# Kernel optimization log

Hardware: AMD Instinct MI355X
Metric: run time of the kernel (lower is better)

## Reference

```python
import jax, jax.numpy as jnp
import numpy as np
from jax import lax

NUM_HEADS = 8
HEAD_DIM = 32
DIM = NUM_HEADS * HEAD_DIM  # 256
SR = 2
B, H, W = 4, 64, 64


def setup_inputs() -> dict:
    key = jax.random.key(0)
    ks = jax.random.split(key, 6)
    x = jax.random.normal(ks[0], (B, DIM, H, W), dtype=jnp.float32)
    # query: 1x1 conv without bias -> plain [out,in] matrix
    Wq = jax.random.normal(ks[1], (DIM, DIM), dtype=jnp.float32) * (1.0 / np.sqrt(DIM))
    # key/value: sr x sr conv, stride sr, no bias (OIHW)
    Wk = jax.random.normal(ks[2], (DIM, DIM, SR, SR), dtype=jnp.float32) * (1.0 / np.sqrt(DIM * SR * SR))
    Wv = jax.random.normal(ks[3], (DIM, DIM, SR, SR), dtype=jnp.float32) * (1.0 / np.sqrt(DIM * SR * SR))
    rel_h = jax.random.normal(ks[4], (1, NUM_HEADS, HEAD_DIM, 1, H // SR), dtype=jnp.float32)
    rel_w = jax.random.normal(ks[5], (1, NUM_HEADS, HEAD_DIM, W // SR, 1), dtype=jnp.float32)
    return {"x": x, "Wq": Wq, "Wk": Wk, "Wv": Wv, "rel_h": rel_h, "rel_w": rel_w}


def reference(x, Wq, Wk, Wv, rel_h, rel_w):
    b, c, h, w = x.shape
    nh, hd = NUM_HEADS, HEAD_DIM
    scale = hd ** (-0.5)
    dn = ('NCHW', 'OIHW', 'NCHW')

    # q: 1x1 conv == channel matmul; [B, C, H*W] -> [B, nh, hd, Nq]
    q = jnp.einsum('oc,bchw->bohw', Wq, x).reshape(b, nh, hd, h * w)
    # k, v: sr x sr conv, stride sr -> [B, nh, hd, Nkv]
    k = lax.conv_general_dilated(x, Wk, window_strides=(SR, SR), padding='VALID',
                                 dimension_numbers=dn).reshape(b, nh, hd, -1)
    v = lax.conv_general_dilated(x, Wv, window_strides=(SR, SR), padding='VALID',
                                 dimension_numbers=dn).reshape(b, nh, hd, -1)

    # attn scores: q^T k -> [B, nh, Nq, Nkv]
    attn = jnp.einsum('bhdn,bhdm->bhnm', q, k)
    # relative positional bias: (rel_h + rel_w) broadcast -> [nh, hd, Nkv]
    pos = (rel_h + rel_w).reshape(nh, hd, -1)
    attn = attn + jnp.einsum('bhdn,hdm->bhnm', q, pos)
    attn = jax.nn.softmax(attn * scale, axis=-1)

    # out = v @ attn^T -> [B, nh, hd, Nq] -> [B, C, H, W]
    out = jnp.einsum('bhdm,bhnm->bhdn', v, attn).reshape(b, c, h, w)
    return out
```

## Files before the change

kernel.cpp:

```cpp
#include <hip/hip_runtime.h>
#include <math.h>


typedef __bf16 bf16;
typedef __attribute__((ext_vector_type(4))) __bf16 bf16x4;
typedef __attribute__((ext_vector_type(8))) __bf16 bf16x8;
typedef __attribute__((ext_vector_type(4))) float f32x4;
typedef __attribute__((ext_vector_type(2))) __fp16 fp16x2_raw;
typedef __attribute__((ext_vector_type(4))) _Float16 f16x4;

#define MFMA16 __builtin_amdgcn_mfma_f32_16x16x32_bf16
#define MFMA16H __builtin_amdgcn_mfma_f32_16x16x16f16

#define QSCALE 0.25503486f
#define SOFTMAX_SHIFT 10.0f

__global__ void k_prep_w(const float* __restrict__ Wq, const float* __restrict__ Wk,
                         const float* __restrict__ Wv,
                         bf16* __restrict__ Wq_bf, bf16* __restrict__ Wkv_bf) {
    int tid = blockIdx.x * 256 + threadIdx.x;
    int c = tid >> 8, i = tid & 255;
    const float* Wsrc = (c < 256) ? Wk : Wv;
    int cs = c & 255;
    f32x4 w4 = ((const f32x4*)Wsrc)[cs * 256 + i];
#pragma unroll
    for (int tap = 0; tap < 4; tap++)
        Wkv_bf[c * 1024 + tap * 256 + i] = (bf16)w4[tap];
    if (tid < 16384) {
        f32x4 q4 = ((const f32x4*)Wq)[tid];
        bf16x4 o;
#pragma unroll
        for (int e = 0; e < 4; e++) o[e] = (bf16)(q4[e] * QSCALE);
        *(bf16x4*)(Wq_bf + tid * 4) = o;
    }
}

__global__ void k_xT(const float* __restrict__ x, bf16* __restrict__ xT) {
    int b = blockIdx.z, c0 = blockIdx.y * 64, n0 = blockIdx.x * 64;
    __shared__ float tile[64][65];
    int t = threadIdx.x;
    const float* xp = x + (size_t)(b * 256 + c0) * 4096 + n0;
#pragma unroll
    for (int k2 = 0; k2 < 16; k2++) {
        int flat = k2 * 256 + t;
        int row = flat >> 6, col = flat & 63;
        tile[row][col] = xp[(size_t)row * 4096 + col];
    }
    __syncthreads();
    bf16* op = xT + (size_t)(b * 4096 + n0) * 256 + c0;
#pragma unroll
    for (int k2 = 0; k2 < 16; k2++) {
        int flat = k2 * 256 + t;
        int row = flat >> 6, col = flat & 63;
        op[(size_t)row * 256 + col] = (bf16)tile[col][row];
    }
}

__launch_bounds__(256)
__global__ void k_gemm_kv(const bf16* __restrict__ xT, const bf16* __restrict__ Wkv_bf,
                          const float* __restrict__ rel_h, const float* __restrict__ rel_w,
                          bf16* __restrict__ kpos_t, _Float16* __restrict__ v_td) {
    int b = blockIdx.z;
    int bx = blockIdx.x;
    int m0 = bx * 32;
    int c0w = blockIdx.y * 64 + (threadIdx.x >> 6) * 16;
    int t = threadIdx.x, l = t & 63;
    int lr = l & 15, lg = l >> 4;
    __shared__ __align__(16) bf16 Ps[2][32 * 264];
    const bf16* xb = xT + (size_t)b * 4096 * 256;
    int srow = t >> 3;
    int scu0 = (t & 7) * 4;
    uint4 pre[4];
#define LOAD_CHUNK(tap)                                                        \
    {                                                                          \
        int dy = (tap) >> 1, dx = (tap) & 1;                                   \
        const bf16* src = xb + (size_t)((2 * bx + dy) * 64 + 2 * srow + dx) * 256; \
        _Pragma("unroll")                                                      \
        for (int j = 0; j < 4; j++)                                            \
            pre[j] = *(const uint4*)(src + (scu0 + j) * 8);                    \
    }
#define WRITE_CHUNK(buf)                                                       \
    {                                                                          \
        bf16* dst = Ps[buf] + srow * 264 + scu0 * 8;                           \
        _Pragma("unroll")                                                      \
        for (int j = 0; j < 4; j++) *(uint4*)(dst + j * 8) = pre[j];           \
    }
    LOAD_CHUNK(0)
    WRITE_CHUNK(0)
    const bf16* Gkb = Wkv_bf + (size_t)(c0w + lr) * 1024 + lg * 8;
    const bf16* Gvb = Gkb + 256 * 1024;
    f32x4 accK[2] = {}, accV[2] = {};
    for (int ch = 0; ch < 4; ch++) {
        if (ch < 3) LOAD_CHUNK(ch + 1)
        __syncthreads();
        const bf16* P = Ps[ch & 1];
#pragma unroll
        for (int kk = 0; kk < 8; kk++) {
            bf16x8 pa0 = *(const bf16x8*)(P + lr * 264 + kk * 32 + lg * 8);
            bf16x8 pa1 = *(const bf16x8*)(P + (16 + lr) * 264 + kk * 32 + lg * 8);
            bf16x8 gk = *(const bf16x8*)(Gkb + ch * 256 + kk * 32);
            bf16x8 gv = *(const bf16x8*)(Gvb + ch * 256 + kk * 32);
            accK[0] = MFMA16(pa0, gk, accK[0], 0, 0, 0);
            accK[1] = MFMA16(pa1, gk, accK[1], 0, 0, 0);
            accV[0] = MFMA16(gv, pa0, accV[0], 0, 0, 0);
            accV[1] = MFMA16(gv, pa1, accV[1], 0, 0, 0);
        }
        if (ch < 3) {
            __syncthreads();
            WRITE_CHUNK((ch + 1) & 1)
        }
    }
    {
        int cc = c0w + lr;
        float rw = rel_w[cc * 32 + bx];
#pragma unroll
        for (int i = 0; i < 2; i++)
#pragma unroll
            for (int r = 0; r < 4; r++) {
                int ml = i * 16 + lg * 4 + r;
                float val = accK[i][r] + rw + rel_h[cc * 32 + ml];
                kpos_t[((size_t)(b * 8 + (cc >> 5)) * 1024 + m0 + ml) * 32 + (cc & 31)] = (bf16)val;
            }
    }
#pragma unroll
    for (int j = 0; j < 2; j++) {
        int m = m0 + j * 16 + lr;
#pragma unroll
        for (int r = 0; r < 4; r++) {
            int cc = c0w + lg * 4 + r;
            v_td[((size_t)(b * 8 + (cc >> 5)) * 32 + (cc & 31)) * 1024 + m] = (_Float16)accV[j][r];
        }
    }
#undef LOAD_CHUNK
#undef WRITE_CHUNK
}

__launch_bounds__(512, 8)
__global__ void k_attn(const bf16* __restrict__ xT, const bf16* __restrict__ Wq_bf,
                       const bf16* __restrict__ kpos_t, const _Float16* __restrict__ v_td,
                       float* __restrict__ out) {
    int b = blockIdx.z, h = blockIdx.y;
    int t = threadIdx.x;
    int w = t >> 6, l = t & 63;
    int n0 = blockIdx.x * 128 + w * 16;
    int lr = l & 15, lg = l >> 4;
    const size_t bh = (size_t)(b * 8 + h);
    __shared__ __align__(16) char smem[2 * 128 * 32 * 2 + 2 * 32 * 136 * 2];
    bf16* KsB = (bf16*)smem;
    _Float16* VsB = (_Float16*)(smem + 16384);
    const bf16* Kb = kpos_t + bh * 1024 * 32;
    const _Float16* Vb = v_td + bh * 32 * 1024;
    uint4 pk_r, pv_r;
#define LOADCH(ch)                                                             \
    {                                                                          \
        pk_r = ((const uint4*)(Kb + (size_t)(ch) * 128 * 32))[t];              \
        pv_r = *(const uint4*)(Vb + (size_t)(t >> 4) * 1024 + (ch) * 128 +     \
                               (t & 15) * 8);                                  \
    }
#define WRITECH(buf)                                                           \
    {                                                                          \
        int m = t >> 2;                                                        \
        int phys = ((m >> 1) + (t & 3)) & 3;                                   \
        *(uint4*)(&KsB[(buf) * 4096 + m * 32 + phys * 8]) = pk_r;              \
        *(uint4*)(&VsB[(buf) * (32 * 136) + (t >> 4) * 136 + (t & 15) * 8]) = pv_r; \
    }
    LOADCH(0)
    bf16* Qs = (bf16*)smem + w * 1280;
    bf16x8 bq0;
    {
        const bf16* Aw = Wq_bf + (size_t)(h * 32 + lr) * 256 + lg * 8;
        const bf16* Bx = xT + (size_t)(b * 4096 + n0 + lr) * 256 + lg * 8;
        f32x4 aq[2] = {};
#pragma unroll
        for (int kk = 0; kk < 8; kk++) {
            bf16x8 a0 = *(const bf16x8*)(Aw + kk * 32);
            bf16x8 a1 = *(const bf16x8*)(Aw + 16 * 256 + kk * 32);
            bf16x8 b0 = *(const bf16x8*)(Bx + kk * 32);
            aq[0] = MFMA16(a0, b0, aq[0], 0, 0, 0);
            aq[1] = MFMA16(a1, b0, aq[1], 0, 0, 0);
        }
#pragma unroll
        for (int i = 0; i < 2; i++) {
            bf16x4 pk;
#pragma unroll
            for (int r = 0; r < 4; r++) pk[r] = (bf16)aq[i][r];
            *(bf16x4*)(Qs + lr * 40 + i * 16 + lg * 4) = pk;
        }
        bf16x4 a0 = *(const bf16x4*)(Qs + lr * 40 + lg * 8);
        bf16x4 a1 = *(const bf16x4*)(Qs + lr * 40 + lg * 8 + 4);
#pragma unroll
        for (int e = 0; e < 4; e++) { bq0[e] = a0[e]; bq0[4 + e] = a1[e]; }
    }
    __syncthreads();
    WRITECH(0)
    LOADCH(1)
    __syncthreads();
    f32x4 accO[2] = {};
    f32x4 accS = {};
    const f16x4 onesv = {(_Float16)1.f, (_Float16)1.f, (_Float16)1.f, (_Float16)1.f};
    const f32x4 zs = {-SOFTMAX_SHIFT, -SOFTMAX_SHIFT, -SOFTMAX_SHIFT, -SOFTMAX_SHIFT};
    const int koff = (((lr >> 1) + lg) & 3) * 8;
    for (int ch = 0; ch < 8; ch++) {
        const bf16* Kc = KsB + (ch & 1) * 4096;
        const _Float16* Vc = VsB + (ch & 1) * (32 * 136);
        __builtin_amdgcn_s_setprio(1);
#pragma unroll
        for (int tt = 0; tt < 8; tt++) {
            bf16x8 ak = *(const bf16x8*)(Kc + (tt * 16 + lr) * 32 + koff);
            f32x4 s0 = MFMA16(ak, bq0, zs, 0, 0, 0);
            f16x4 p0;
            {
                fp16x2_raw c01 = __builtin_amdgcn_cvt_pkrtz(
                    __builtin_amdgcn_exp2f(s0[0]), __builtin_amdgcn_exp2f(s0[1]));
                fp16x2_raw c23 = __builtin_amdgcn_cvt_pkrtz(
                    __builtin_amdgcn_exp2f(s0[2]), __builtin_amdgcn_exp2f(s0[3]));
                p0[0] = c01[0]; p0[1] = c01[1]; p0[2] = c23[0]; p0[3] = c23[1];
            }
            f16x4 v0 = *(const f16x4*)(Vc + lr * 136 + tt * 16 + lg * 4);
            f16x4 v1 = *(const f16x4*)(Vc + (16 + lr) * 136 + tt * 16 + lg * 4);
            accO[0] = MFMA16H(p0, v0, accO[0], 0, 0, 0);
            accO[1] = MFMA16H(p0, v1, accO[1], 0, 0, 0);
            accS    = MFMA16H(p0, onesv, accS, 0, 0, 0);
        }
        __builtin_amdgcn_s_setprio(0);
        if (ch < 7) {
            WRITECH((ch + 1) & 1)
            if (ch < 6) LOADCH(ch + 2)
            __syncthreads();
        }
    }
#undef LOADCH
#undef WRITECH
    float inv[4];
#pragma unroll
    for (int r = 0; r < 4; r++) inv[r] = 1.0f / accS[r];
#pragma unroll
    for (int dt = 0; dt < 2; dt++) {
        int c = h * 32 + dt * 16 + lr;
        float* op = out + (size_t)(b * 256 + c) * 4096 + n0 + lg * 4;
        f32x4 o;
#pragma unroll
        for (int r = 0; r < 4; r++) o[r] = accO[dt][r] * inv[r];
        *(f32x4*)op = o;
    }
}

extern "C" void kernel_launch(void* const* d_in, const int* in_sizes, int n_in,
                              void* d_out, int out_size, void* d_ws, size_t ws_size,
                              hipStream_t stream) {
    const float* x    = (const float*)d_in[0];
    const float* Wq   = (const float*)d_in[1];
    const float* Wk   = (const float*)d_in[2];
    const float* Wv   = (const float*)d_in[3];
    const float* relh = (const float*)d_in[4];
    const float* relw = (const float*)d_in[5];
    float* out = (float*)d_out;
    char* ws = (char*)d_ws;

    bf16*      xT     = (bf16*)(ws);
    bf16*      kposT  = (bf16*)(ws + (8u << 20));
    _Float16*  v_td   = (_Float16*)(ws + (10u << 20));
    bf16*      Wq_bf  = (bf16*)(ws + (12u << 20));
    bf16*      Wkv_bf = (bf16*)(ws + (12u << 20) + (256u << 10));

    k_prep_w <<<512,            256, 0, stream>>>(Wq, Wk, Wv, Wq_bf, Wkv_bf);
    k_xT     <<<dim3(64, 4, 4), 256, 0, stream>>>(x, xT);
    k_gemm_kv<<<dim3(32, 4, 4), 256, 0, stream>>>(xT, Wkv_bf, relh, relw, kposT, v_td);
    k_attn   <<<dim3(32, 8, 4), 512, 0, stream>>>(xT, Wq_bf, kposT, v_td, out);
}
```

Measured before the change: 146.5 us.

## Vectorize prep and transpose memory ops, halve gemm_kv tile for more blocks

```diff
diff --git a/kernel.cpp b/kernel.cpp
--- a/kernel.cpp
+++ b/kernel.cpp
@@ -19,19 +19,28 @@
                          const float* __restrict__ Wv,
                          bf16* __restrict__ Wq_bf, bf16* __restrict__ Wkv_bf) {
     int tid = blockIdx.x * 256 + threadIdx.x;
-    int c = tid >> 8, i = tid & 255;
-    const float* Wsrc = (c < 256) ? Wk : Wv;
-    int cs = c & 255;
-    f32x4 w4 = ((const f32x4*)Wsrc)[cs * 256 + i];
-#pragma unroll
-    for (int tap = 0; tap < 4; tap++)
-        Wkv_bf[c * 1024 + tap * 256 + i] = (bf16)w4[tap];
-    if (tid < 16384) {
-        f32x4 q4 = ((const f32x4*)Wq)[tid];
+    if (tid < 32768) {
+        int c = tid >> 6, i4 = (tid & 63) * 4;
+        const float* Wsrc = (c < 256) ? Wk : Wv;
+        int cs = c & 255;
+        f32x4 r[4];
+#pragma unroll
+        for (int j = 0; j < 4; j++)
+            r[j] = ((const f32x4*)Wsrc)[cs * 256 + i4 + j];
+#pragma unroll
+        for (int tap = 0; tap < 4; tap++) {
+            bf16x4 o;
+#pragma unroll
+            for (int j = 0; j < 4; j++) o[j] = (bf16)r[j][tap];
+            *(bf16x4*)(Wkv_bf + c * 1024 + tap * 256 + i4) = o;
+        }
+    } else {
+        int q = tid - 32768;
+        f32x4 q4 = ((const f32x4*)Wq)[q];
         bf16x4 o;
 #pragma unroll
         for (int e = 0; e < 4; e++) o[e] = (bf16)(q4[e] * QSCALE);
-        *(bf16x4*)(Wq_bf + tid * 4) = o;
+        *(bf16x4*)(Wq_bf + q * 4) = o;
     }
 }
 
@@ -41,18 +50,23 @@
     int t = threadIdx.x;
     const float* xp = x + (size_t)(b * 256 + c0) * 4096 + n0;
 #pragma unroll
-    for (int k2 = 0; k2 < 16; k2++) {
-        int flat = k2 * 256 + t;
-        int row = flat >> 6, col = flat & 63;
-        tile[row][col] = xp[(size_t)row * 4096 + col];
+    for (int it = 0; it < 4; it++) {
+        int u = it * 256 + t;
+        int row = u >> 4, colq = u & 15;
+        f32x4 v = *(const f32x4*)(xp + (size_t)row * 4096 + colq * 4);
+#pragma unroll
+        for (int e = 0; e < 4; e++) tile[row][colq * 4 + e] = v[e];
     }
     __syncthreads();
     bf16* op = xT + (size_t)(b * 4096 + n0) * 256 + c0;
 #pragma unroll
-    for (int k2 = 0; k2 < 16; k2++) {
-        int flat = k2 * 256 + t;
-        int row = flat >> 6, col = flat & 63;
-        op[(size_t)row * 256 + col] = (bf16)tile[col][row];
+    for (int it = 0; it < 2; it++) {
+        int u = it * 256 + t;
+        int orow = u >> 3, oc8 = (u & 7) * 8;
+        bf16x8 o;
+#pragma unroll
+        for (int e = 0; e < 8; e++) o[e] = (bf16)tile[oc8 + e][orow];
+        *(bf16x8*)(op + (size_t)orow * 256 + oc8) = o;
     }
 }
 
@@ -62,48 +76,46 @@
                           bf16* __restrict__ kpos_t, _Float16* __restrict__ v_td) {
     int b = blockIdx.z;
     int bx = blockIdx.x;
-    int m0 = bx * 32;
+    int m0 = bx * 16;
     int c0w = blockIdx.y * 64 + (threadIdx.x >> 6) * 16;
     int t = threadIdx.x, l = t & 63;
     int lr = l & 15, lg = l >> 4;
-    __shared__ __align__(16) bf16 Ps[2][32 * 264];
+    __shared__ __align__(16) bf16 Ps[2][16 * 264];
     const bf16* xb = xT + (size_t)b * 4096 * 256;
-    int srow = t >> 3;
-    int scu0 = (t & 7) * 4;
-    uint4 pre[4];
+    int srow = t >> 4;
+    int scu0 = (t & 15) * 2;
+    uint4 pre[2];
 #define LOAD_CHUNK(tap)                                                        \
     {                                                                          \
         int dy = (tap) >> 1, dx = (tap) & 1;                                   \
-        const bf16* src = xb + (size_t)((2 * bx + dy) * 64 + 2 * srow + dx) * 256; \
+        const bf16* src = xb + (size_t)((2 * (bx >> 1) + dy) * 64 +            \
+                                        2 * ((bx & 1) * 16 + srow) + dx) * 256;\
         _Pragma("unroll")                                                      \
-        for (int j = 0; j < 4; j++)                                            \
-            pre[j] = *(const uint4*)(src + (scu0 + j) * 8);                    \
+        for (int j = 0; j < 2; j++)                                            \
+            pre[j] = ((const uint4*)src)[scu0 + j];                            \
     }
 #define WRITE_CHUNK(buf)                                                       \
     {                                                                          \
         bf16* dst = Ps[buf] + srow * 264 + scu0 * 8;                           \
         _Pragma("unroll")                                                      \
-        for (int j = 0; j < 4; j++) *(uint4*)(dst + j * 8) = pre[j];           \
+        for (int j = 0; j < 2; j++) *(uint4*)(dst + j * 8) = pre[j];           \
     }
     LOAD_CHUNK(0)
     WRITE_CHUNK(0)
     const bf16* Gkb = Wkv_bf + (size_t)(c0w + lr) * 1024 + lg * 8;
     const bf16* Gvb = Gkb + 256 * 1024;
-    f32x4 accK[2] = {}, accV[2] = {};
+    f32x4 accK = {}, accV = {};
     for (int ch = 0; ch < 4; ch++) {
         if (ch < 3) LOAD_CHUNK(ch + 1)
         __syncthreads();
         const bf16* P = Ps[ch & 1];
 #pragma unroll
         for (int kk = 0; kk < 8; kk++) {
-            bf16x8 pa0 = *(const bf16x8*)(P + lr * 264 + kk * 32 + lg * 8);
-            bf16x8 pa1 = *(const bf16x8*)(P + (16 + lr) * 264 + kk * 32 + lg * 8);
+            bf16x8 pa = *(const bf16x8*)(P + lr * 264 + kk * 32 + lg * 8);
             bf16x8 gk = *(const bf16x8*)(Gkb + ch * 256 + kk * 32);
             bf16x8 gv = *(const bf16x8*)(Gvb + ch * 256 + kk * 32);
-            accK[0] = MFMA16(pa0, gk, accK[0], 0, 0, 0);
-            accK[1] = MFMA16(pa1, gk, accK[1], 0, 0, 0);
-            accV[0] = MFMA16(gv, pa0, accV[0], 0, 0, 0);
-            accV[1] = MFMA16(gv, pa1, accV[1], 0, 0, 0);
+            accK = MFMA16(pa, gk, accK, 0, 0, 0);
+            accV = MFMA16(gv, pa, accV, 0, 0, 0);
         }
         if (ch < 3) {
             __syncthreads();
@@ -112,23 +124,21 @@
     }
     {
         int cc = c0w + lr;
-        float rw = rel_w[cc * 32 + bx];
-#pragma unroll
-        for (int i = 0; i < 2; i++)
-#pragma unroll
-            for (int r = 0; r < 4; r++) {
-                int ml = i * 16 + lg * 4 + r;
-                float val = accK[i][r] + rw + rel_h[cc * 32 + ml];
-                kpos_t[((size_t)(b * 8 + (cc >> 5)) * 1024 + m0 + ml) * 32 + (cc & 31)] = (bf16)val;
-            }
-    }
-#pragma unroll
-    for (int j = 0; j < 2; j++) {
-        int m = m0 + j * 16 + lr;
+        float rw = rel_w[cc * 32 + (bx >> 1)];
+#pragma unroll
+        for (int r = 0; r < 4; r++) {
+            int ml = lg * 4 + r;
+            int mg = (bx & 1) * 16 + ml;
+            float val = accK[r] + rw + rel_h[cc * 32 + mg];
+            kpos_t[((size_t)(b * 8 + (cc >> 5)) * 1024 + m0 + ml) * 32 + (cc & 31)] = (bf16)val;
+        }
+    }
+    {
+        int m = m0 + lr;
 #pragma unroll
         for (int r = 0; r < 4; r++) {
             int cc = c0w + lg * 4 + r;
-            v_td[((size_t)(b * 8 + (cc >> 5)) * 32 + (cc & 31)) * 1024 + m] = (_Float16)accV[j][r];
+            v_td[((size_t)(b * 8 + (cc >> 5)) * 32 + (cc & 31)) * 1024 + m] = (_Float16)accV[r];
         }
     }
 #undef LOAD_CHUNK
@@ -263,8 +273,8 @@
     bf16*      Wq_bf  = (bf16*)(ws + (12u << 20));
     bf16*      Wkv_bf = (bf16*)(ws + (12u << 20) + (256u << 10));
 
-    k_prep_w <<<512,            256, 0, stream>>>(Wq, Wk, Wv, Wq_bf, Wkv_bf);
+    k_prep_w <<<192,            256, 0, stream>>>(Wq, Wk, Wv, Wq_bf, Wkv_bf);
     k_xT     <<<dim3(64, 4, 4), 256, 0, stream>>>(x, xT);
-    k_gemm_kv<<<dim3(32, 4, 4), 256, 0, stream>>>(xT, Wkv_bf, relh, relw, kposT, v_td);
+    k_gemm_kv<<<dim3(64, 4, 4), 256, 0, stream>>>(xT, Wkv_bf, relh, relw, kposT, v_td);
     k_attn   <<<dim3(32, 8, 4), 512, 0, stream>>>(xT, Wq_bf, kposT, v_td, out);
 }
```

Measured after the change: 157.7 us. +7.6%, slower.
